# Optimization experiments

Hardware: AMD Instinct MI355X
Metric: run time of the kernel (lower is better)

## Reference

```python
import jax, jax.numpy as jnp
import numpy as np

HEAD_DIM = 128
PROJ_DIM = 64


def setup_inputs() -> dict:
    key = jax.random.key(0)
    kq, kk, kv, kr = jax.random.split(key, 4)
    B, H, NQ, NKV = 1, 16, 2048, 4096
    Q = jax.random.normal(kq, (B, H, NQ, HEAD_DIM), dtype=jnp.float32)
    K = jax.random.normal(kk, (B, H, NKV, HEAD_DIM), dtype=jnp.float32)
    V = jax.random.normal(kv, (B, H, NKV, HEAD_DIM), dtype=jnp.float32)
    # R ~ N(0,1) / sqrt(proj_dim), as in the torch __init__
    R = jax.random.normal(kr, (HEAD_DIM, PROJ_DIM), dtype=jnp.float32) / (PROJ_DIM ** 0.5)
    return {"Q": Q, "K": K, "V": V, "R": R}


def reference(Q, K, V, R):
    proj_dim = R.shape[-1]
    scale = 1.0 / (proj_dim ** 0.5)
    # Project Q and K into the random-projection space: [B,H,N,proj_dim]
    Q_proj = jnp.einsum('bhnd,dp->bhnp', Q, R)
    K_proj = jnp.einsum('bhmd,dp->bhmp', K, R)
    # scores: [B,H,NQ,NKV]
    scores = jnp.einsum('bhnp,bhmp->bhnm', Q_proj, K_proj) * scale
    weights = jax.nn.softmax(scores, axis=-1)
    # output: [B,H,NQ,head_dim]
    return jnp.einsum('bhnm,bhmd->bhnd', weights, V)
```

## Files before the change

### kernel.cpp

```cpp
#include <hip/hip_runtime.h>

#define HEADS 16
#define NQ    2048
#define NKV   4096
#define DH    128
#define PDIM  64

typedef __bf16 bf16_t;
typedef bf16_t bf16x8 __attribute__((ext_vector_type(8)));
typedef bf16_t bf16x4 __attribute__((ext_vector_type(4)));
typedef bf16_t bf16x2 __attribute__((ext_vector_type(2)));
typedef float  f32x4  __attribute__((ext_vector_type(4)));
typedef float  f32x16 __attribute__((ext_vector_type(16)));
typedef int    i32x4  __attribute__((ext_vector_type(4)));

typedef __attribute__((address_space(3))) unsigned int       lds_u32;
typedef __attribute__((address_space(1))) const unsigned int glb_u32;

__device__ __forceinline__ void dma16(const void* g, void* l) {
  __builtin_amdgcn_global_load_lds((glb_u32*)g, (lds_u32*)l, 16, 0, 0);
}

__global__ __launch_bounds__(256) void prep_kernel(
    const float* __restrict__ Q, const float* __restrict__ K,
    const float* __restrict__ V, const float* __restrict__ R,
    bf16_t* __restrict__ Qp, bf16_t* __restrict__ Kp, bf16_t* __restrict__ Vt)
{
  __shared__ char lds[32768];
  const int tid = threadIdx.x;
  const int bid = blockIdx.x;

  if (bid >= 1536) {
    float* sF = (float*)lds;
    const int vb = bid - 1536;
    const float* tp = V + (long)vb * 64 * DH;
#pragma unroll
    for (int rep = 0; rep < 8; ++rep) {
      const int slot = tid + rep * 256;
      const int j = slot >> 5, g = slot & 31;
      f32x4 v = *(const f32x4*)(tp + j * DH + g * 4);
      *(f32x4*)(&sF[j * 128 + ((g ^ ((j >> 3) & 7)) << 2)]) = v;
    }
    __syncthreads();

    const int h = vb >> 6, jt = vb & 63;
    bf16_t* op = Vt + (long)h * DH * NKV + jt * 64;
#pragma unroll
    for (int rep = 0; rep < 4; ++rep) {
      const int slot = tid + rep * 256;
      const int d = slot >> 3, j8 = (slot & 7) * 8;
      const int key = slot & 7;
      const int gsw = (((d >> 2) ^ key) << 2) + (d & 3);
      bf16x8 w;
#pragma unroll
      for (int jj = 0; jj < 8; ++jj) w[jj] = (bf16_t)sF[(j8 + jj) * 128 + gsw];
      *(bf16x8*)(op + (long)d * NKV + j8) = w;
    }
    return;
  }

  bf16_t* sR = (bf16_t*)lds;
  bf16_t* sYb = (bf16_t*)(lds + 64 * 136 * 2);

  const int isQ = (bid < 512);
  const float* src = isQ ? Q : K;
  const long row0  = isQ ? (long)bid * 64 : (long)(bid - 512) * 64;
  const float scale = isQ ? 0.18033688011112042f : 1.0f;
  bf16_t* Y = isQ ? Qp : Kp;

#pragma unroll
  for (int rep = 0; rep < 32; ++rep) {
    const int idx = tid + rep * 256;
    sR[(idx & 63) * 136 + (idx >> 6)] = (bf16_t)R[idx];
  }
  __syncthreads();

  const int wave = tid >> 6, lane = tid & 63;
  const int n16  = lane & 15, quad = lane >> 4;

  bf16x8 bfr[4][4];
#pragma unroll
  for (int nt = 0; nt < 4; ++nt)
#pragma unroll
    for (int kk = 0; kk < 4; ++kk)
      bfr[nt][kk] = *(const bf16x8*)(sR + (nt * 16 + n16) * 136 + kk * 32 + quad * 8);

  const int arow = wave * 16 + n16;
  const float* xp = src + (row0 + arow) * DH;
  bf16x8 a[4];
#pragma unroll
  for (int kk = 0; kk < 4; ++kk) {
    const int k0 = kk * 32 + quad * 8;
    f32x4 x0 = *(const f32x4*)(xp + k0);
    f32x4 x1 = *(const f32x4*)(xp + k0 + 4);
    bf16x8 av;
#pragma unroll
    for (int j = 0; j < 4; ++j) { av[j] = (bf16_t)(x0[j] * scale); av[4 + j] = (bf16_t)(x1[j] * scale); }
    a[kk] = av;
  }

  bf16_t* sy = sYb + wave * (16 * 72);
#pragma unroll
  for (int nt = 0; nt < 4; ++nt) {
    f32x4 acc = {0.f, 0.f, 0.f, 0.f};
#pragma unroll
    for (int kk = 0; kk < 4; ++kk)
      acc = __builtin_amdgcn_mfma_f32_16x16x32_bf16(a[kk], bfr[nt][kk], acc, 0, 0, 0);
#pragma unroll
    for (int r = 0; r < 4; ++r)
      sy[(quad * 4 + r) * 72 + nt * 16 + n16] = (bf16_t)acc[r];
  }
  const long xrow = row0 + wave * 16;
  const int row = lane >> 2, cg = lane & 3;
  bf16x8 w0 = *(const bf16x8*)(&sy[row * 72 + cg * 16]);
  bf16x8 w1 = *(const bf16x8*)(&sy[row * 72 + cg * 16 + 8]);
  *(bf16x8*)(Y + (xrow + row) * PDIM + cg * 16)     = w0;
  *(bf16x8*)(Y + (xrow + row) * PDIM + cg * 16 + 8) = w1;
}

__global__ __launch_bounds__(128, 2) void flash_kernel(
    const bf16_t* __restrict__ Qp, const bf16_t* __restrict__ Kp,
    const bf16_t* __restrict__ Vt, bf16_t* __restrict__ Opart,
    float* __restrict__ Lpart, float* __restrict__ Out,
    int splits, int iters)
{
  __shared__ char smem[24576];
  bf16_t* sK = (bf16_t*)smem;
  bf16_t* sV = (bf16_t*)(smem + 8192);

  const int tid  = threadIdx.x;
  const int wave = tid >> 6, lane = tid & 63;
  const int l31  = lane & 31, h = lane >> 5;

  const int head = blockIdx.x & 15;
  const int qt   = (blockIdx.x >> 4) & 15;
  const int sp   = blockIdx.x >> 8;

  const int qbase = qt * 128 + wave * 64;
  const int kv0   = sp * (64 * iters);

  bf16x8 qf[2][4];
#pragma unroll
  for (int qsub = 0; qsub < 2; ++qsub)
#pragma unroll
    for (int k = 0; k < 4; ++k)
      qf[qsub][k] = *(const bf16x8*)(Qp + ((long)head * NQ + qbase + qsub * 32 + l31) * PDIM
                                     + k * 16 + h * 8);

  f32x16 o[2][4] = {};
  float rsum[2] = {0.f, 0.f};

  const bf16_t* kpH = Kp + (long)head * NKV * PDIM;
  const bf16_t* vtH = Vt + (long)head * DH * NKV;

  const int sw = ((lane & 7) ^ ((lane >> 3) & 7)) * 8;
  const int r8 = lane >> 3;

  for (int t = 0; t < iters; ++t) {
    const int kvb = kv0 + t * 64;
    __syncthreads();
    if (wave == 0) {
#pragma unroll
      for (int i = 0; i < 8; ++i)
        dma16(kpH + (long)(kvb + i * 8 + r8) * PDIM + sw, smem + i * 1024);
#pragma unroll
      for (int i = 0; i < 4; ++i)
        dma16(vtH + (long)(i * 8 + r8) * NKV + kvb + sw, smem + 8192 + i * 1024);
    } else {
#pragma unroll
      for (int i = 4; i < 16; ++i)
        dma16(vtH + (long)(i * 8 + r8) * NKV + kvb + sw, smem + 8192 + i * 1024);
    }
    __syncthreads();

#pragma unroll
    for (int s = 0; s < 2; ++s) {
      int bfr[2][2][4];
#pragma unroll
      for (int qsub = 0; qsub < 2; ++qsub) {
        f32x16 sc = {};
        const int r = s * 32 + l31;
#pragma unroll
        for (int k = 0; k < 4; ++k) {
          const int c = 2 * k + h;
          const bf16x8 a = *(const bf16x8*)(sK + r * 64 + ((c ^ (r & 7)) * 8));
          sc = __builtin_amdgcn_mfma_f32_32x32x16_bf16(a, qf[qsub][k], sc, 0, 0, 0);
        }
        int pk[4][2];
#pragma unroll
        for (int rg = 0; rg < 4; ++rg) {
          const float p0 = __builtin_amdgcn_exp2f(sc[rg * 4 + 0]);
          const float p1 = __builtin_amdgcn_exp2f(sc[rg * 4 + 1]);
          const float p2 = __builtin_amdgcn_exp2f(sc[rg * 4 + 2]);
          const float p3 = __builtin_amdgcn_exp2f(sc[rg * 4 + 3]);
          rsum[qsub] += (p0 + p1) + (p2 + p3);
          union { bf16x2 v; int i; } u0, u1;
          u0.v = bf16x2{(bf16_t)p0, (bf16_t)p1};
          u1.v = bf16x2{(bf16_t)p2, (bf16_t)p3};
          pk[rg][0] = u0.i; pk[rg][1] = u1.i;
        }
#pragma unroll
        for (int cl = 0; cl < 2; ++cl) {
          const int e00 = __shfl_xor(pk[2 * cl][0], 32);
          const int e01 = __shfl_xor(pk[2 * cl][1], 32);
          const int e10 = __shfl_xor(pk[2 * cl + 1][0], 32);
          const int e11 = __shfl_xor(pk[2 * cl + 1][1], 32);
          bfr[qsub][cl][0] = h ? e10 : pk[2 * cl][0];
          bfr[qsub][cl][1] = h ? e11 : pk[2 * cl][1];
          bfr[qsub][cl][2] = h ? pk[2 * cl + 1][0] : e00;
          bfr[qsub][cl][3] = h ? pk[2 * cl + 1][1] : e01;
        }
      }
#pragma unroll
      for (int dsub = 0; dsub < 4; ++dsub) {
        const int r = dsub * 32 + l31;
#pragma unroll
        for (int cl = 0; cl < 2; ++cl) {
          const int c = 2 * (2 * s + cl) + h;
          const bf16x8 va = *(const bf16x8*)(sV + r * 64 + ((c ^ (r & 7)) * 8));
#pragma unroll
          for (int qsub = 0; qsub < 2; ++qsub) {
            union { i32x4 i; bf16x8 v; } pb;
            pb.i = i32x4{bfr[qsub][cl][0], bfr[qsub][cl][1],
                         bfr[qsub][cl][2], bfr[qsub][cl][3]};
            o[qsub][dsub] = __builtin_amdgcn_mfma_f32_32x32x16_bf16(va, pb.v, o[qsub][dsub], 0, 0, 0);
          }
        }
      }
    }
  }

  __syncthreads();
  bf16_t* myT = (bf16_t*)(smem + wave * 8704);
#pragma unroll
  for (int qsub = 0; qsub < 2; ++qsub) {
    const float lsum = rsum[qsub] + __shfl_xor(rsum[qsub], 32);
    const float scale = (splits > 1) ? 1.0f : (1.0f / lsum);
#pragma unroll
    for (int dsub = 0; dsub < 4; ++dsub)
#pragma unroll
      for (int rg = 0; rg < 4; ++rg) {
        bf16x4 w = { (bf16_t)(o[qsub][dsub][rg * 4 + 0] * scale),
                     (bf16_t)(o[qsub][dsub][rg * 4 + 1] * scale),
                     (bf16_t)(o[qsub][dsub][rg * 4 + 2] * scale),
                     (bf16_t)(o[qsub][dsub][rg * 4 + 3] * scale) };
        *(bf16x4*)(myT + l31 * 136 + dsub * 32 + rg * 8 + h * 4) = w;
      }
    const int qglob = qbase + qsub * 32;
#pragma unroll
    for (int j = 0; j < 8; ++j) {
      const int ql = j * 4 + (lane >> 4);
      bf16x8 v = *(const bf16x8*)(myT + ql * 136 + (lane & 15) * 8);
      if (splits > 1) {
        *(bf16x8*)(Opart + (((long)sp * HEADS + head) * NQ + qglob + ql) * DH + (lane & 15) * 8) = v;
      } else {
        float* op = Out + ((long)head * NQ + qglob + ql) * DH + (lane & 15) * 8;
        f32x4 a = {(float)v[0], (float)v[1], (float)v[2], (float)v[3]};
        f32x4 b = {(float)v[4], (float)v[5], (float)v[6], (float)v[7]};
        *(f32x4*)op = a; *(f32x4*)(op + 4) = b;
      }
    }
    if (splits > 1 && h == 0)
      Lpart[((long)sp * HEADS + head) * NQ + qglob + l31] = lsum;
  }
}

__global__ __launch_bounds__(256) void combine_kernel(
    const bf16_t* __restrict__ Opart, const float* __restrict__ Lpart,
    float* __restrict__ Out)
{
  const long idx = (long)blockIdx.x * 256 + threadIdx.x;
  const int  d8  = (int)(idx & 15);
  const long hq  = idx >> 4;
  float l = 0.f;
  float acc[8];
#pragma unroll
  for (int j = 0; j < 8; ++j) acc[j] = 0.f;
#pragma unroll
  for (int s = 0; s < 4; ++s) {
    l += Lpart[s * (long)(HEADS * NQ) + hq];
    bf16x8 v = *(const bf16x8*)(Opart + (s * (long)(HEADS * NQ) + hq) * DH + d8 * 8);
#pragma unroll
    for (int j = 0; j < 8; ++j) acc[j] += (float)v[j];
  }
  const float inv = 1.f / l;
  f32x4 o0 = { acc[0] * inv, acc[1] * inv, acc[2] * inv, acc[3] * inv };
  f32x4 o1 = { acc[4] * inv, acc[5] * inv, acc[6] * inv, acc[7] * inv };
  float* op = Out + hq * DH + d8 * 8;
  *(f32x4*)(op)     = o0;
  *(f32x4*)(op + 4) = o1;
}

extern "C" void kernel_launch(void* const* d_in, const int* in_sizes, int n_in,
                              void* d_out, int out_size, void* d_ws, size_t ws_size,
                              hipStream_t stream)
{
  const float* Q = (const float*)d_in[0];
  const float* K = (const float*)d_in[1];
  const float* V = (const float*)d_in[2];
  const float* R = (const float*)d_in[3];
  float* Out = (float*)d_out;

  char* ws = (char*)d_ws;
  bf16_t* Qp = (bf16_t*)(ws);
  bf16_t* Kp = (bf16_t*)(ws + (size_t)(4  << 20));
  bf16_t* Vt = (bf16_t*)(ws + (size_t)(12 << 20));
  bf16_t* Opart = (bf16_t*)(ws + (size_t)(28 << 20));
  float*  Lpart = (float*)(ws + (size_t)(60 << 20));

  const size_t need4 = (size_t)(60 << 20) + 4ull * HEADS * NQ * sizeof(float);
  const int splits = (ws_size >= need4) ? 4 : 1;
  const int iters  = NKV / (64 * splits);

  prep_kernel<<<2560, 256, 0, stream>>>(Q, K, V, R, Qp, Kp, Vt);
  flash_kernel<<<splits * 256, 128, 0, stream>>>(Qp, Kp, Vt, Opart, Lpart, Out,
                                                 splits, iters);
  if (splits == 4)
    combine_kernel<<<2048, 256, 0, stream>>>(Opart, Lpart, Out);
}
```

Before: 194.1 us.

## Split flash block across four waves with 32 query rows each

Each flash block now uses 256 threads (four waves), each wave owning 32 query rows instead of two waves owning 64. Per-wave accumulators and Q fragments are halved, launch bounds become (256,3), and the K/V DMA loads are spread over four waves. LDS grows to hold four per-wave output transpose buffers. The aim is more waves in flight for latency hiding, at the cost of each wave reusing every K/V tile read from LDS over fewer query rows.

```diff
diff --git a/kernel.cpp b/kernel.cpp
--- a/kernel.cpp
+++ b/kernel.cpp
@@ -118,13 +118,13 @@
   *(bf16x8*)(Y + (xrow + row) * PDIM + cg * 16 + 8) = w1;
 }
 
-__global__ __launch_bounds__(128, 2) void flash_kernel(
+__global__ __launch_bounds__(256, 3) void flash_kernel(
     const bf16_t* __restrict__ Qp, const bf16_t* __restrict__ Kp,
     const bf16_t* __restrict__ Vt, bf16_t* __restrict__ Opart,
     float* __restrict__ Lpart, float* __restrict__ Out,
     int splits, int iters)
 {
-  __shared__ char smem[24576];
+  __shared__ char smem[34816];
   bf16_t* sK = (bf16_t*)smem;
   bf16_t* sV = (bf16_t*)(smem + 8192);
 
@@ -136,19 +136,17 @@
   const int qt   = (blockIdx.x >> 4) & 15;
   const int sp   = blockIdx.x >> 8;
 
-  const int qbase = qt * 128 + wave * 64;
+  const int qbase = qt * 128 + wave * 32;
   const int kv0   = sp * (64 * iters);
 
-  bf16x8 qf[2][4];
-#pragma unroll
-  for (int qsub = 0; qsub < 2; ++qsub)
-#pragma unroll
-    for (int k = 0; k < 4; ++k)
-      qf[qsub][k] = *(const bf16x8*)(Qp + ((long)head * NQ + qbase + qsub * 32 + l31) * PDIM
-                                     + k * 16 + h * 8);
-
-  f32x16 o[2][4] = {};
-  float rsum[2] = {0.f, 0.f};
+  bf16x8 qf[4];
+#pragma unroll
+  for (int k = 0; k < 4; ++k)
+    qf[k] = *(const bf16x8*)(Qp + ((long)head * NQ + qbase + l31) * PDIM
+                             + k * 16 + h * 8);
+
+  f32x16 o[4] = {};
+  float rsum = 0.f;
 
   const bf16_t* kpH = Kp + (long)head * NKV * PDIM;
   const bf16_t* vtH = Vt + (long)head * DH * NKV;
@@ -161,108 +159,105 @@
     __syncthreads();
     if (wave == 0) {
 #pragma unroll
-      for (int i = 0; i < 8; ++i)
+      for (int i = 0; i < 6; ++i)
+        dma16(kpH + (long)(kvb + i * 8 + r8) * PDIM + sw, smem + i * 1024);
+    } else if (wave == 1) {
+#pragma unroll
+      for (int i = 6; i < 8; ++i)
         dma16(kpH + (long)(kvb + i * 8 + r8) * PDIM + sw, smem + i * 1024);
 #pragma unroll
       for (int i = 0; i < 4; ++i)
         dma16(vtH + (long)(i * 8 + r8) * NKV + kvb + sw, smem + 8192 + i * 1024);
+    } else if (wave == 2) {
+#pragma unroll
+      for (int i = 4; i < 10; ++i)
+        dma16(vtH + (long)(i * 8 + r8) * NKV + kvb + sw, smem + 8192 + i * 1024);
     } else {
 #pragma unroll
-      for (int i = 4; i < 16; ++i)
+      for (int i = 10; i < 16; ++i)
         dma16(vtH + (long)(i * 8 + r8) * NKV + kvb + sw, smem + 8192 + i * 1024);
     }
     __syncthreads();
 
 #pragma unroll
     for (int s = 0; s < 2; ++s) {
-      int bfr[2][2][4];
-#pragma unroll
-      for (int qsub = 0; qsub < 2; ++qsub) {
-        f32x16 sc = {};
-        const int r = s * 32 + l31;
-#pragma unroll
-        for (int k = 0; k < 4; ++k) {
-          const int c = 2 * k + h;
-          const bf16x8 a = *(const bf16x8*)(sK + r * 64 + ((c ^ (r & 7)) * 8));
-          sc = __builtin_amdgcn_mfma_f32_32x32x16_bf16(a, qf[qsub][k], sc, 0, 0, 0);
-        }
-        int pk[4][2];
-#pragma unroll
-        for (int rg = 0; rg < 4; ++rg) {
-          const float p0 = __builtin_amdgcn_exp2f(sc[rg * 4 + 0]);
-          const float p1 = __builtin_amdgcn_exp2f(sc[rg * 4 + 1]);
-          const float p2 = __builtin_amdgcn_exp2f(sc[rg * 4 + 2]);
-          const float p3 = __builtin_amdgcn_exp2f(sc[rg * 4 + 3]);
-          rsum[qsub] += (p0 + p1) + (p2 + p3);
-          union { bf16x2 v; int i; } u0, u1;
-          u0.v = bf16x2{(bf16_t)p0, (bf16_t)p1};
-          u1.v = bf16x2{(bf16_t)p2, (bf16_t)p3};
-          pk[rg][0] = u0.i; pk[rg][1] = u1.i;
-        }
+      f32x16 sc = {};
+      const int r = s * 32 + l31;
+#pragma unroll
+      for (int k = 0; k < 4; ++k) {
+        const int c = 2 * k + h;
+        const bf16x8 a = *(const bf16x8*)(sK + r * 64 + ((c ^ (r & 7)) * 8));
+        sc = __builtin_amdgcn_mfma_f32_32x32x16_bf16(a, qf[k], sc, 0, 0, 0);
+      }
+      int pk[4][2];
+#pragma unroll
+      for (int rg = 0; rg < 4; ++rg) {
+        const float p0 = __builtin_amdgcn_exp2f(sc[rg * 4 + 0]);
+        const float p1 = __builtin_amdgcn_exp2f(sc[rg * 4 + 1]);
+        const float p2 = __builtin_amdgcn_exp2f(sc[rg * 4 + 2]);
+        const float p3 = __builtin_amdgcn_exp2f(sc[rg * 4 + 3]);
+        rsum += (p0 + p1) + (p2 + p3);
+        union { bf16x2 v; int i; } u0, u1;
+        u0.v = bf16x2{(bf16_t)p0, (bf16_t)p1};
+        u1.v = bf16x2{(bf16_t)p2, (bf16_t)p3};
+        pk[rg][0] = u0.i; pk[rg][1] = u1.i;
+      }
+      int bfr[2][4];
+#pragma unroll
+      for (int cl = 0; cl < 2; ++cl) {
+        const int e00 = __shfl_xor(pk[2 * cl][0], 32);
+        const int e01 = __shfl_xor(pk[2 * cl][1], 32);
+        const int e10 = __shfl_xor(pk[2 * cl + 1][0], 32);
+        const int e11 = __shfl_xor(pk[2 * cl + 1][1], 32);
+        bfr[cl][0] = h ? e10 : pk[2 * cl][0];
+        bfr[cl][1] = h ? e11 : pk[2 * cl][1];
+        bfr[cl][2] = h ? pk[2 * cl + 1][0] : e00;
+        bfr[cl][3] = h ? pk[2 * cl + 1][1] : e01;
+      }
+#pragma unroll
+      for (int dsub = 0; dsub < 4; ++dsub) {
+        const int rr = dsub * 32 + l31;
 #pragma unroll
         for (int cl = 0; cl < 2; ++cl) {
-          const int e00 = __shfl_xor(pk[2 * cl][0], 32);
-          const int e01 = __shfl_xor(pk[2 * cl][1], 32);
-          const int e10 = __shfl_xor(pk[2 * cl + 1][0], 32);
-          const int e11 = __shfl_xor(pk[2 * cl + 1][1], 32);
-          bfr[qsub][cl][0] = h ? e10 : pk[2 * cl][0];
-          bfr[qsub][cl][1] = h ? e11 : pk[2 * cl][1];
-          bfr[qsub][cl][2] = h ? pk[2 * cl + 1][0] : e00;
-          bfr[qsub][cl][3] = h ? pk[2 * cl + 1][1] : e01;
+          const int c = 2 * (2 * s + cl) + h;
+          const bf16x8 va = *(const bf16x8*)(sV + rr * 64 + ((c ^ (rr & 7)) * 8));
+          union { i32x4 i; bf16x8 v; } pb;
+          pb.i = i32x4{bfr[cl][0], bfr[cl][1], bfr[cl][2], bfr[cl][3]};
+          o[dsub] = __builtin_amdgcn_mfma_f32_32x32x16_bf16(va, pb.v, o[dsub], 0, 0, 0);
         }
       }
-#pragma unroll
-      for (int dsub = 0; dsub < 4; ++dsub) {
-        const int r = dsub * 32 + l31;
-#pragma unroll
-        for (int cl = 0; cl < 2; ++cl) {
-          const int c = 2 * (2 * s + cl) + h;
-          const bf16x8 va = *(const bf16x8*)(sV + r * 64 + ((c ^ (r & 7)) * 8));
-#pragma unroll
-          for (int qsub = 0; qsub < 2; ++qsub) {
-            union { i32x4 i; bf16x8 v; } pb;
-            pb.i = i32x4{bfr[qsub][cl][0], bfr[qsub][cl][1],
-                         bfr[qsub][cl][2], bfr[qsub][cl][3]};
-            o[qsub][dsub] = __builtin_amdgcn_mfma_f32_32x32x16_bf16(va, pb.v, o[qsub][dsub], 0, 0, 0);
-          }
-        }
-      }
     }
   }
 
   __syncthreads();
   bf16_t* myT = (bf16_t*)(smem + wave * 8704);
-#pragma unroll
-  for (int qsub = 0; qsub < 2; ++qsub) {
-    const float lsum = rsum[qsub] + __shfl_xor(rsum[qsub], 32);
-    const float scale = (splits > 1) ? 1.0f : (1.0f / lsum);
-#pragma unroll
-    for (int dsub = 0; dsub < 4; ++dsub)
-#pragma unroll
-      for (int rg = 0; rg < 4; ++rg) {
-        bf16x4 w = { (bf16_t)(o[qsub][dsub][rg * 4 + 0] * scale),
-                     (bf16_t)(o[qsub][dsub][rg * 4 + 1] * scale),
-                     (bf16_t)(o[qsub][dsub][rg * 4 + 2] * scale),
-                     (bf16_t)(o[qsub][dsub][rg * 4 + 3] * scale) };
-        *(bf16x4*)(myT + l31 * 136 + dsub * 32 + rg * 8 + h * 4) = w;
-      }
-    const int qglob = qbase + qsub * 32;
-#pragma unroll
-    for (int j = 0; j < 8; ++j) {
-      const int ql = j * 4 + (lane >> 4);
-      bf16x8 v = *(const bf16x8*)(myT + ql * 136 + (lane & 15) * 8);
-      if (splits > 1) {
-        *(bf16x8*)(Opart + (((long)sp * HEADS + head) * NQ + qglob + ql) * DH + (lane & 15) * 8) = v;
-      } else {
-        float* op = Out + ((long)head * NQ + qglob + ql) * DH + (lane & 15) * 8;
-        f32x4 a = {(float)v[0], (float)v[1], (float)v[2], (float)v[3]};
-        f32x4 b = {(float)v[4], (float)v[5], (float)v[6], (float)v[7]};
-        *(f32x4*)op = a; *(f32x4*)(op + 4) = b;
-      }
-    }
-    if (splits > 1 && h == 0)
-      Lpart[((long)sp * HEADS + head) * NQ + qglob + l31] = lsum;
-  }
+  const float lsum = rsum + __shfl_xor(rsum, 32);
+  const float scale = (splits > 1) ? 1.0f : (1.0f / lsum);
+#pragma unroll
+  for (int dsub = 0; dsub < 4; ++dsub)
+#pragma unroll
+    for (int rg = 0; rg < 4; ++rg) {
+      bf16x4 w = { (bf16_t)(o[dsub][rg * 4 + 0] * scale),
+                   (bf16_t)(o[dsub][rg * 4 + 1] * scale),
+                   (bf16_t)(o[dsub][rg * 4 + 2] * scale),
+                   (bf16_t)(o[dsub][rg * 4 + 3] * scale) };
+      *(bf16x4*)(myT + l31 * 136 + dsub * 32 + rg * 8 + h * 4) = w;
+    }
+#pragma unroll
+  for (int j = 0; j < 8; ++j) {
+    const int ql = j * 4 + (lane >> 4);
+    bf16x8 v = *(const bf16x8*)(myT + ql * 136 + (lane & 15) * 8);
+    if (splits > 1) {
+      *(bf16x8*)(Opart + (((long)sp * HEADS + head) * NQ + qbase + ql) * DH + (lane & 15) * 8) = v;
+    } else {
+      float* op = Out + ((long)head * NQ + qbase + ql) * DH + (lane & 15) * 8;
+      f32x4 a = {(float)v[0], (float)v[1], (float)v[2], (float)v[3]};
+      f32x4 b = {(float)v[4], (float)v[5], (float)v[6], (float)v[7]};
+      *(f32x4*)op = a; *(f32x4*)(op + 4) = b;
+    }
+  }
+  if (splits > 1 && h == 0)
+    Lpart[((long)sp * HEADS + head) * NQ + qbase + l31] = lsum;
 }
 
 __global__ __launch_bounds__(256) void combine_kernel(
@@ -313,7 +308,7 @@
   const int iters  = NKV / (64 * splits);
 
   prep_kernel<<<2560, 256, 0, stream>>>(Q, K, V, R, Qp, Kp, Vt);
-  flash_kernel<<<splits * 256, 128, 0, stream>>>(Qp, Kp, Vt, Opart, Lpart, Out,
+  flash_kernel<<<splits * 256, 256, 0, stream>>>(Qp, Kp, Vt, Opart, Lpart, Out,
                                                  splits, iters);
   if (splits == 4)
     combine_kernel<<<2048, 256, 0, stream>>>(Opart, Lpart, Out);
```

Measured after the change: 189.7 us. -2.2%, faster.
